# Kernel optimization log

Hardware: AMD Instinct MI355X
Metric: run time of the kernel (lower is better)

The kernel has to match this reference:

```python
import jax, jax.numpy as jnp
import numpy as np

N = 100000      # nodes
E = 1600000     # edges (avg degree 16)
DIN = 128
DOUT = 128


def setup_inputs() -> dict:
    key = jax.random.key(0)
    k1, k2, k3, k4 = jax.random.split(key, 4)
    x = jax.random.normal(k1, (N, DIN), dtype=jnp.float32)
    # destination rows: ensure every node appears at least once so the
    # bincount-based degree normalization never divides by zero
    row = jnp.concatenate([jnp.arange(N, dtype=jnp.int32),
                           jax.random.randint(k2, (E - N,), 0, N, dtype=jnp.int32)])
    col = jax.random.randint(k3, (E,), 0, N, dtype=jnp.int32)
    edge_index = jnp.stack([row, col])  # [2, E]
    # reset_parameters: weight ~ U(-stdv, stdv), stdv = 6/sqrt(in+out); bias = 0
    stdv = 6.0 / np.sqrt(DIN + DOUT)
    W = jax.random.uniform(k4, (DIN, DOUT), dtype=jnp.float32, minval=-stdv, maxval=stdv)
    bias = jnp.zeros((DOUT,), dtype=jnp.float32)
    alpha = jnp.full((DOUT,), 0.25, dtype=jnp.float32)  # PReLU per-channel init
    return {"x": x, "W": W, "bias": bias, "alpha": alpha,
            "edge_index": edge_index, "activation": 0}


def reference(x, W, bias, alpha, edge_index, activation):
    n = x.shape[0]
    support = x @ W                                   # [N, DOUT]
    row, col = edge_index[0], edge_index[1]
    # output.index_add_(0, row, support[col])
    agg = jax.ops.segment_sum(support[col], row, num_segments=n)   # [N, DOUT]
    # degree = bincount(row, minlength=N)
    deg = jax.ops.segment_sum(jnp.ones((row.shape[0],), support.dtype), row,
                              num_segments=n)[:, None]             # [N, 1]
    out = agg / deg
    d10 = support.shape[1] // 10
    h = jnp.concatenate([out[:, :d10], support[:, d10:]], axis=1) + bias
    # PReLU with per-channel alpha
    return jnp.where(h >= 0, h, alpha * h)
```

## Files before the change

kernel.cpp:

```cpp
#include <hip/hip_runtime.h>

#define DIM 128
#define D10 12

typedef __attribute__((ext_vector_type(8))) short bf16x8;
typedef __attribute__((ext_vector_type(4))) float f32x4;

__device__ __forceinline__ void fma4(float4& a, float s, const float4& w) {
    a.x = fmaf(s, w.x, a.x);
    a.y = fmaf(s, w.y, a.y);
    a.z = fmaf(s, w.z, a.z);
    a.w = fmaf(s, w.w, a.w);
}

__device__ __forceinline__ unsigned short f2bf(float f) {
    union { float f; unsigned int u; } v; v.f = f;
    unsigned int u = v.u;
    unsigned int r = (u + 0x7FFFu + ((u >> 16) & 1u)) >> 16;
    return (unsigned short)r;
}

__device__ __forceinline__ float bf2f(unsigned int hi16) {
    union { unsigned int u; float f; } v; v.u = hi16 << 16;
    return v.f;
}

__device__ __forceinline__ void atomPkAddBf16(unsigned int* p, unsigned int v) {
    unsigned long long a = (unsigned long long)p;
    asm volatile("global_atomic_pk_add_bf16 %0, %1, off" :: "v"(a), "v"(v) : "memory");
}

__device__ __forceinline__ void atomAddF32(float* p, float v) {
    unsafeAtomicAdd(p, v);
}


__global__ void k_wt(const float* __restrict__ W, unsigned short* __restrict__ Wt) {
    int i = blockIdx.x * 256 + threadIdx.x;
    if (i >= DIM * DIM) return;
    int k = i >> 7, nn = i & 127;
    Wt[nn * DIM + k] = f2bf(W[i]);
}


__global__ __launch_bounds__(256) void k_gemm(
    const float4* __restrict__ xv, float* __restrict__ out,
    const uint4* __restrict__ Wtv,
    const float* __restrict__ bias, const float* __restrict__ alpha,
    unsigned int* __restrict__ s12b, int n)
{
    __shared__ alignas(16) char lds[48 * 1024];
    char* xs  = lds;
    char* wsm = lds + 16384;

    int tid = threadIdx.x;
    int rowbase = blockIdx.x * 64;

#pragma unroll
    for (int ii = 0; ii < 8; ++ii) {
        int i = tid + ii * 256;
        int nn = i >> 4, kq = i & 15;
        uint4 v = Wtv[nn * 16 + kq];
        int byte = (nn * 256 + kq * 16) ^ ((nn & 7) << 4);
        *reinterpret_cast<uint4*>(wsm + byte) = v;
    }
#pragma unroll
    for (int ii = 0; ii < 8; ++ii) {
        int i = tid + ii * 256;
        int lr = i >> 5, c4 = i & 31;
        int r = rowbase + lr;
        float4 v; v.x = v.y = v.z = v.w = 0.f;
        if (r < n) v = xv[(size_t)r * 32 + c4];
        uint2 p;
        p.x = (unsigned int)f2bf(v.x) | ((unsigned int)f2bf(v.y) << 16);
        p.y = (unsigned int)f2bf(v.z) | ((unsigned int)f2bf(v.w) << 16);
        int byte = (lr * 256 + c4 * 8) ^ ((lr & 7) << 4);
        *reinterpret_cast<uint2*>(xs + byte) = p;
    }
    __syncthreads();

    int wv = tid >> 6;
    int lane = tid & 63;
    int lr0 = wv * 16;
    int arow = lr0 + (lane & 15);
    int kgrp = (lane >> 4) * 8;

    f32x4 acc[8];
#pragma unroll
    for (int t = 0; t < 8; ++t) acc[t] = (f32x4){0.f, 0.f, 0.f, 0.f};

#pragma unroll
    for (int kb = 0; kb < 4; ++kb) {
        int koff = kb * 32 + kgrp;
        int abyte = (arow * 256 + koff * 2) ^ ((arow & 7) << 4);
        bf16x8 a = *reinterpret_cast<const bf16x8*>(xs + abyte);
#pragma unroll
        for (int t = 0; t < 8; ++t) {
            int c = t * 16 + (lane & 15);
            int bbyte = (c * 256 + koff * 2) ^ ((c & 7) << 4);
            bf16x8 b = *reinterpret_cast<const bf16x8*>(wsm + bbyte);
            acc[t] = __builtin_amdgcn_mfma_f32_16x16x32_bf16(a, b, acc[t], 0, 0, 0);
        }
    }

    int colbase = lane & 15;
    int rgrp = (lane >> 4) * 4;
    float bi[8], al[8];
#pragma unroll
    for (int t = 0; t < 8; ++t) {
        int c = t * 16 + colbase;
        bi[t] = bias[c];
        al[t] = alpha[c];
    }
#pragma unroll
    for (int j = 0; j < 4; ++j) {
        int r = rowbase + lr0 + rgrp + j;
        if (r >= n) continue;
#pragma unroll
        for (int t = 0; t < 8; ++t) {
            int c = t * 16 + colbase;
            float h = acc[t][j];
            if (t == 0 && colbase < D10) {
                float h1 = __shfl_xor(h, 1, 64);
                if ((colbase & 1) == 0) {
                    unsigned int pk = (unsigned int)f2bf(h) |
                                      ((unsigned int)f2bf(h1) << 16);
                    s12b[(size_t)r * 6 + (colbase >> 1)] = pk;
                }
            } else {
                h += bi[t];
                h = h >= 0.f ? h : al[t] * h;
                out[(size_t)r * DIM + c] = h;
            }
        }
    }
}


__global__ void k_edge_agg(const unsigned int* __restrict__ s12b,
                           const int* __restrict__ row, const int* __restrict__ col,
                           long long total, unsigned int* __restrict__ agg) {
    long long i = (long long)blockIdx.x * blockDim.x + threadIdx.x;
    long long stride = (long long)gridDim.x * blockDim.x;
    for (long long g = i; g < total; g += stride) {
        int e = (int)(g >> 3), l = (int)(g & 7);
        if (l < 7) {
            int r = row[e];
            unsigned int v;
            if (l < 6) v = s12b[(size_t)col[e] * 6 + l];
            else       v = 0x00003F80u;
            atomPkAddBf16(&agg[(size_t)r * 8 + l], v);
        }
    }
}


__global__ void k_epi12(const uint4* __restrict__ aggv, const float* __restrict__ bias,
                        const float* __restrict__ alpha, float* __restrict__ out, int n) {
    int r = blockIdx.x * blockDim.x + threadIdx.x;
    if (r >= n) return;
    uint4 a0 = aggv[(size_t)r * 2];
    uint4 a1 = aggv[(size_t)r * 2 + 1];
    float dg = bf2f(a1.z & 0xFFFFu);
    float invd = 1.f / (dg >= 1.f ? dg : 1.f);
    unsigned int s[6] = {a0.x, a0.y, a0.z, a0.w, a1.x, a1.y};
    float h[12];
#pragma unroll
    for (int q = 0; q < 6; ++q) {
        h[2 * q]     = bf2f(s[q] & 0xFFFFu) * invd + bias[2 * q];
        h[2 * q + 1] = bf2f(s[q] >> 16)     * invd + bias[2 * q + 1];
    }
#pragma unroll
    for (int c = 0; c < 12; ++c) {
        float v = h[c];
        h[c] = v >= 0.f ? v : alpha[c] * v;
    }
    float4* o = reinterpret_cast<float4*>(out + (size_t)r * DIM);
    o[0] = make_float4(h[0], h[1], h[2], h[3]);
    o[1] = make_float4(h[4], h[5], h[6], h[7]);
    o[2] = make_float4(h[8], h[9], h[10], h[11]);
}


__global__ void k_count_deg(const int* __restrict__ row, int E, int* __restrict__ deg) {
    int i = blockIdx.x * blockDim.x + threadIdx.x;
    int stride = gridDim.x * blockDim.x;
    for (; i < E; i += stride) atomicAdd(&deg[row[i]], 1);
}

__global__ void k_edge_atomic(const float4* __restrict__ xv, const int* __restrict__ row,
                              const int* __restrict__ col, int E, float* __restrict__ out) {
    int i = blockIdx.x * blockDim.x + threadIdx.x;
    int stride = gridDim.x * blockDim.x;
    int total = E * 32;
    for (; i < total; i += stride) {
        int e = i >> 5, lane = i & 31;
        int r = row[e], c = col[e];
        float4 v = xv[(size_t)c * 32 + lane];
        float* dst = out + (size_t)r * DIM + lane * 4;
        atomAddF32(dst + 0, v.x);
        atomAddF32(dst + 1, v.y);
        atomAddF32(dst + 2, v.z);
        atomAddF32(dst + 3, v.w);
    }
}

__global__ __launch_bounds__(256) void k_final_legacy(const float4* __restrict__ xv,
                                                      float4* __restrict__ outv,
                                                      const float4* __restrict__ Wv,
                                                      const float4* __restrict__ biasv,
                                                      const float4* __restrict__ alphav,
                                                      const int* __restrict__ deg, int n) {
    __shared__ float4 Ws4[DIM * 32];
    __shared__ float4 vs4[2][32 * 32];

    int tid = threadIdx.x;
    int rowbase = blockIdx.x * 32;
    if (rowbase >= n) return;

    for (int i = tid; i < DIM * 32; i += 256) Ws4[i] = Wv[i];
    for (int i = tid; i < 32 * 32; i += 256) {
        int r = rowbase + (i >> 5);
        if (r < n) {
            vs4[0][i] = outv[(size_t)r * 32 + (i & 31)];
            vs4[1][i] = xv[(size_t)r * 32 + (i & 31)];
        }
    }
    __syncthreads();

    int tx = tid & 31;
    int ty = tid >> 5;
    int r0 = ty * 4;
    const float4* V = (tx < (D10 / 4)) ? vs4[0] : vs4[1];

    float4 acc[4];
#pragma unroll
    for (int r = 0; r < 4; r++) { acc[r].x = acc[r].y = acc[r].z = acc[r].w = 0.f; }

#pragma unroll 8
    for (int k4 = 0; k4 < 32; k4++) {
        float4 w0 = Ws4[(k4 * 4 + 0) * 32 + tx];
        float4 w1 = Ws4[(k4 * 4 + 1) * 32 + tx];
        float4 w2 = Ws4[(k4 * 4 + 2) * 32 + tx];
        float4 w3 = Ws4[(k4 * 4 + 3) * 32 + tx];
#pragma unroll
        for (int r = 0; r < 4; r++) {
            float4 v = V[(r0 + r) * 32 + k4];
            fma4(acc[r], v.x, w0); fma4(acc[r], v.y, w1);
            fma4(acc[r], v.z, w2); fma4(acc[r], v.w, w3);
        }
    }

    float4 b4 = biasv[tx];
    float4 a4 = alphav[tx];
#pragma unroll
    for (int r = 0; r < 4; r++) {
        int row = rowbase + r0 + r;
        if (row >= n) continue;
        float4 h = acc[r];
        if (tx < (D10 / 4)) {
            int d = deg[row];
            float invd = 1.0f / (float)(d > 0 ? d : 1);
            h.x *= invd; h.y *= invd; h.z *= invd; h.w *= invd;
        }
        h.x += b4.x; h.y += b4.y; h.z += b4.z; h.w += b4.w;
        h.x = h.x >= 0.f ? h.x : a4.x * h.x;
        h.y = h.y >= 0.f ? h.y : a4.y * h.y;
        h.z = h.z >= 0.f ? h.z : a4.z * h.z;
        h.w = h.w >= 0.f ? h.w : a4.w * h.w;
        outv[(size_t)row * 32 + tx] = h;
    }
}


extern "C" void kernel_launch(void* const* d_in, const int* in_sizes, int n_in,
                              void* d_out, int out_size, void* d_ws, size_t ws_size,
                              hipStream_t stream) {
    const float* x     = (const float*)d_in[0];
    const float* W     = (const float*)d_in[1];
    const float* bias  = (const float*)d_in[2];
    const float* alpha = (const float*)d_in[3];
    const int*   ei    = (const int*)d_in[4];

    int N = in_sizes[0] / DIM;
    int E = in_sizes[4] / 2;
    const int* row = ei;
    const int* col = ei + E;
    float* out = (float*)d_out;

    int gemm_blocks = (N + 63) / 64;
    size_t wt_bytes = (size_t)DIM * DIM * 2;

    size_t need_A = wt_bytes + (size_t)(6 + 8) * N * 4;
    size_t need_E = (size_t)N * 4;

    if (ws_size >= need_A) {
        unsigned short* Wt   = (unsigned short*)d_ws;
        unsigned int* s12b   = (unsigned int*)((char*)d_ws + wt_bytes);
        unsigned int* agg    = s12b + (size_t)6 * N;

        hipMemsetAsync(agg, 0, (size_t)8 * N * sizeof(unsigned int), stream);
        k_wt<<<(DIM * DIM + 255) / 256, 256, 0, stream>>>(W, Wt);
        k_gemm<<<gemm_blocks, 256, 0, stream>>>((const float4*)x, out, (const uint4*)Wt,
                                                bias, alpha, s12b, N);
        long long total = (long long)E * 8;
        k_edge_agg<<<4096, 256, 0, stream>>>(s12b, row, col, total, agg);
        k_epi12<<<(N + 255) / 256, 256, 0, stream>>>((const uint4*)agg, bias, alpha, out, N);
    } else if (ws_size >= need_E) {
        int* deg = (int*)d_ws;
        hipMemsetAsync(out, 0, (size_t)N * DIM * sizeof(float), stream);
        hipMemsetAsync(deg, 0, (size_t)N * sizeof(int), stream);
        k_count_deg<<<2048, 256, 0, stream>>>(row, E, deg);
        k_edge_atomic<<<4096, 256, 0, stream>>>((const float4*)x, row, col, E, out);
        k_final_legacy<<<(N + 31) / 32, 256, 0, stream>>>((const float4*)x, (float4*)out,
                                                          (const float4*)W, (const float4*)bias,
                                                          (const float4*)alpha, deg, N);
    }
}
```

Baseline: 119.9 us.

## Split 12-column support into separate kernel and co-schedule GEMM with edge aggregation

```diff
diff --git a/kernel.cpp b/kernel.cpp
--- a/kernel.cpp
+++ b/kernel.cpp
@@ -43,27 +43,83 @@
 }
 
 
-__global__ __launch_bounds__(256) void k_gemm(
+__global__ __launch_bounds__(256) void k_s12(const float4* __restrict__ xv,
+                                             const float4* __restrict__ Wv,
+                                             unsigned int* __restrict__ s12b, int n) {
+    __shared__ float4 xsf[64 * 33];
+    __shared__ float4 w12[128 * 3];
+
+    int tid = threadIdx.x;
+    int rowbase = blockIdx.x * 64;
+
+    for (int i = tid; i < 128 * 3; i += 256) {
+        int k = i / 3, q = i - k * 3;
+        w12[i] = Wv[k * 32 + q];
+    }
+    for (int i = tid; i < 64 * 32; i += 256) {
+        int r = rowbase + (i >> 5);
+        float4 v; v.x = v.y = v.z = v.w = 0.f;
+        if (r < n) v = xv[(size_t)r * 32 + (i & 31)];
+        xsf[(i >> 5) * 33 + (i & 31)] = v;
+    }
+    __syncthreads();
+
+    if (tid < 192) {
+        int lrow = tid / 3;
+        int q = tid - lrow * 3;
+        const float4* xr = &xsf[lrow * 33];
+        float4 acc; acc.x = acc.y = acc.z = acc.w = 0.f;
+#pragma unroll 4
+        for (int k4 = 0; k4 < 32; ++k4) {
+            float4 v = xr[k4];
+            float4 w0 = w12[(k4 * 4 + 0) * 3 + q];
+            float4 w1 = w12[(k4 * 4 + 1) * 3 + q];
+            float4 w2 = w12[(k4 * 4 + 2) * 3 + q];
+            float4 w3 = w12[(k4 * 4 + 3) * 3 + q];
+            fma4(acc, v.x, w0); fma4(acc, v.y, w1);
+            fma4(acc, v.z, w2); fma4(acc, v.w, w3);
+        }
+        int grow = rowbase + lrow;
+        if (grow < n) {
+            unsigned int p0 = (unsigned int)f2bf(acc.x) | ((unsigned int)f2bf(acc.y) << 16);
+            unsigned int p1 = (unsigned int)f2bf(acc.z) | ((unsigned int)f2bf(acc.w) << 16);
+            s12b[(size_t)grow * 6 + 2 * q]     = p0;
+            s12b[(size_t)grow * 6 + 2 * q + 1] = p1;
+        }
+    }
+}
+
+
+__global__ __launch_bounds__(256) void k_fat(
     const float4* __restrict__ xv, float* __restrict__ out,
     const uint4* __restrict__ Wtv,
     const float* __restrict__ bias, const float* __restrict__ alpha,
-    unsigned int* __restrict__ s12b, int n)
+    const unsigned int* __restrict__ s12b,
+    const int* __restrict__ row, const int* __restrict__ col,
+    unsigned int* __restrict__ agg,
+    int gemmBlocks, long long aggTotal, int n)
 {
-    __shared__ alignas(16) char lds[48 * 1024];
-    char* xs  = lds;
-    char* wsm = lds + 16384;
+    __shared__ alignas(16) char xs[16 * 1024];
+
+    if ((int)blockIdx.x >= gemmBlocks) {
+        int aggBlocks = gridDim.x - gemmBlocks;
+        long long i = (long long)((int)blockIdx.x - gemmBlocks) * 256 + threadIdx.x;
+        long long stride = (long long)aggBlocks * 256;
+        for (long long g = i; g < aggTotal; g += stride) {
+            int e = (int)(g >> 3), l = (int)(g & 7);
+            if (l < 7) {
+                int r = row[e];
+                unsigned int v = (l < 6) ? s12b[(size_t)col[e] * 6 + l]
+                                         : 0x00003F80u;
+                atomPkAddBf16(&agg[(size_t)r * 8 + l], v);
+            }
+        }
+        return;
+    }
 
     int tid = threadIdx.x;
     int rowbase = blockIdx.x * 64;
 
-#pragma unroll
-    for (int ii = 0; ii < 8; ++ii) {
-        int i = tid + ii * 256;
-        int nn = i >> 4, kq = i & 15;
-        uint4 v = Wtv[nn * 16 + kq];
-        int byte = (nn * 256 + kq * 16) ^ ((nn & 7) << 4);
-        *reinterpret_cast<uint4*>(wsm + byte) = v;
-    }
 #pragma unroll
     for (int ii = 0; ii < 8; ++ii) {
         int i = tid + ii * 256;
@@ -85,6 +141,8 @@
     int arow = lr0 + (lane & 15);
     int kgrp = (lane >> 4) * 8;
 
+    const char* Wb = reinterpret_cast<const char*>(Wtv);
+
     f32x4 acc[8];
 #pragma unroll
     for (int t = 0; t < 8; ++t) acc[t] = (f32x4){0.f, 0.f, 0.f, 0.f};
@@ -97,8 +155,7 @@
 #pragma unroll
         for (int t = 0; t < 8; ++t) {
             int c = t * 16 + (lane & 15);
-            int bbyte = (c * 256 + koff * 2) ^ ((c & 7) << 4);
-            bf16x8 b = *reinterpret_cast<const bf16x8*>(wsm + bbyte);
+            bf16x8 b = *reinterpret_cast<const bf16x8*>(Wb + (c * DIM + koff) * 2);
             acc[t] = __builtin_amdgcn_mfma_f32_16x16x32_bf16(a, b, acc[t], 0, 0, 0);
         }
     }
@@ -119,37 +176,11 @@
 #pragma unroll
         for (int t = 0; t < 8; ++t) {
             int c = t * 16 + colbase;
+            if (t == 0 && colbase < D10) continue;
             float h = acc[t][j];
-            if (t == 0 && colbase < D10) {
-                float h1 = __shfl_xor(h, 1, 64);
-                if ((colbase & 1) == 0) {
-                    unsigned int pk = (unsigned int)f2bf(h) |
-                                      ((unsigned int)f2bf(h1) << 16);
-                    s12b[(size_t)r * 6 + (colbase >> 1)] = pk;
-                }
-            } else {
-                h += bi[t];
-                h = h >= 0.f ? h : al[t] * h;
-                out[(size_t)r * DIM + c] = h;
-            }
-        }
-    }
-}
-
-
-__global__ void k_edge_agg(const unsigned int* __restrict__ s12b,
-                           const int* __restrict__ row, const int* __restrict__ col,
-                           long long total, unsigned int* __restrict__ agg) {
-    long long i = (long long)blockIdx.x * blockDim.x + threadIdx.x;
-    long long stride = (long long)gridDim.x * blockDim.x;
-    for (long long g = i; g < total; g += stride) {
-        int e = (int)(g >> 3), l = (int)(g & 7);
-        if (l < 7) {
-            int r = row[e];
-            unsigned int v;
-            if (l < 6) v = s12b[(size_t)col[e] * 6 + l];
-            else       v = 0x00003F80u;
-            atomPkAddBf16(&agg[(size_t)r * 8 + l], v);
+            h += bi[t];
+            h = h >= 0.f ? h : al[t] * h;
+            out[(size_t)r * DIM + c] = h;
         }
     }
 }
@@ -288,7 +319,8 @@
     const int* col = ei + E;
     float* out = (float*)d_out;
 
-    int gemm_blocks = (N + 63) / 64;
+    int gemmBlocks = (N + 63) / 64;
+    int aggBlocks  = 2048;
     size_t wt_bytes = (size_t)DIM * DIM * 2;
 
     size_t need_A = wt_bytes + (size_t)(6 + 8) * N * 4;
@@ -301,10 +333,12 @@
 
         hipMemsetAsync(agg, 0, (size_t)8 * N * sizeof(unsigned int), stream);
         k_wt<<<(DIM * DIM + 255) / 256, 256, 0, stream>>>(W, Wt);
-        k_gemm<<<gemm_blocks, 256, 0, stream>>>((const float4*)x, out, (const uint4*)Wt,
-                                                bias, alpha, s12b, N);
-        long long total = (long long)E * 8;
-        k_edge_agg<<<4096, 256, 0, stream>>>(s12b, row, col, total, agg);
+        k_s12<<<gemmBlocks, 256, 0, stream>>>((const float4*)x, (const float4*)W,
+                                              s12b, N);
+        long long aggTotal = (long long)E * 8;
+        k_fat<<<gemmBlocks + aggBlocks, 256, 0, stream>>>(
+            (const float4*)x, out, (const uint4*)Wt, bias, alpha,
+            s12b, row, col, agg, gemmBlocks, aggTotal, N);
         k_epi12<<<(N + 255) / 256, 256, 0, stream>>>((const uint4*)agg, bias, alpha, out, N);
     } else if (ws_size >= need_E) {
         int* deg = (int*)d_ws;
```

New measurement: 146.2 us. +22.0%, slower.
